# Optimization experiments

Hardware: AMD Instinct MI355X
Metric: run time of the kernel (lower is better)

Reference implementation:

```python
import jax, jax.numpy as jnp
import numpy as np

NUM_HEADS = 12

def setup_inputs() -> dict:
    key = jax.random.key(0)
    ks = jax.random.split(key, 8)
    B, C, H, W = 16, 512, 64, 64
    T = 768
    s = 0.02
    return {
        "cond": jax.random.normal(ks[0], (B, C, H, W), jnp.float32),
        "t": jax.random.normal(ks[1], (B, T), jnp.float32),
        "Wk": jax.random.normal(ks[2], (T, C), jnp.float32) * s,
        "bk": jax.random.normal(ks[3], (T,), jnp.float32) * s,
        "Wv": jax.random.normal(ks[4], (T, C), jnp.float32) * s,
        "bv": jax.random.normal(ks[5], (T,), jnp.float32) * s,
        "Wo": jax.random.normal(ks[6], (C, T), jnp.float32) * s,
        "bo": jax.random.normal(ks[7], (C,), jnp.float32) * s,
    }

def reference(cond, t, Wk, bk, Wv, bv, Wo, bo):
    B, C, H, W = cond.shape
    T = Wk.shape[0]
    h = NUM_HEADS
    d = T // h
    HW = H * W
    x = cond.reshape(B, C, HW)                                  # [B,C,HW]
    # 1x1 convs == channel GEMMs
    k = (jnp.einsum('tc,bcm->btm', Wk, x) + bk[None, :, None]).reshape(B, h, d, HW)
    v = (jnp.einsum('tc,bcm->btm', Wv, x) + bv[None, :, None]).reshape(B, h, d, HW)
    q = t.reshape(B, h, d)                                      # single query per head
    scale = d ** 0.5
    attn = jax.nn.softmax(jnp.einsum('bhd,bhdm->bhm', q, k) / scale, axis=-1)
    out = jnp.einsum('bhm,bhdm->bhd', attn, v).reshape(B, T)    # [B,T]
    out = jnp.einsum('ct,bt->bc', Wo, out) + bo                 # out_proj on (B,T,1,1)
    out = out[:, :, None, None]                                 # broadcast over H,W
    return out + cond
```

## Files before the change

kernel.cpp:

```cpp
#include <hip/hip_runtime.h>
#include <math.h>

#define B_   16
#define C_   512
#define HW_  4096
#define T_   768
#define NH   12
#define DH   64

typedef float nfloat4 __attribute__((ext_vector_type(4)));


__global__ __launch_bounds__(512) void qk_kernel(
    const float* __restrict__ t, const float* __restrict__ Wk,
    const float* __restrict__ bk, float* __restrict__ qkT,
    float* __restrict__ qb) {
  int bh = blockIdx.x;
  int b = bh / NH, h = bh % NH;
  __shared__ float tl[DH];
  int tid = threadIdx.x;
  if (tid < DH) tl[tid] = t[b * T_ + h * DH + tid];
  __syncthreads();
  int c = tid;
  float acc = 0.f;
#pragma unroll
  for (int dd = 0; dd < DH; ++dd)
    acc += tl[dd] * Wk[(h * DH + dd) * C_ + c];
  qkT[((size_t)b * C_ + c) * NH + h] = acc * 0.125f;
  if (tid == 0) {
    float s = 0.f;
    for (int dd = 0; dd < DH; ++dd) s += tl[dd] * bk[h * DH + dd];
    qb[bh] = s * 0.125f;
  }
}

template <int CS>
__global__ __launch_bounds__(128) void s_kernel(
    const float* __restrict__ x, const float* __restrict__ qkT,
    float* __restrict__ sp) {
  constexpr int CB = C_ / CS;
  int mt = blockIdx.x;
  int cs = blockIdx.y;
  int b  = blockIdx.z;
  int tid = threadIdx.x;

  __shared__ float qc[CB * NH];
  const float* src = qkT + ((size_t)b * C_ + cs * CB) * NH;
  for (int i = tid; i < CB * NH; i += 128) qc[i] = src[i];
  __syncthreads();

  int m0 = mt * 512 + tid * 4;
  float4 acc[NH];
#pragma unroll
  for (int h = 0; h < NH; ++h) acc[h] = make_float4(0.f, 0.f, 0.f, 0.f);

  const float* xb = x + (size_t)b * C_ * HW_ + (size_t)(cs * CB) * HW_ + m0;
  for (int c0 = 0; c0 < CB; c0 += 16) {
    float4 xv[16];
#pragma unroll
    for (int j = 0; j < 16; ++j)
      xv[j] = *(const float4*)(xb + (size_t)(c0 + j) * HW_);
#pragma unroll
    for (int j = 0; j < 16; ++j) {
      const float* q = qc + (c0 + j) * NH;
#pragma unroll
      for (int h = 0; h < NH; ++h) {
        float qh = q[h];
        acc[h].x += qh * xv[j].x; acc[h].y += qh * xv[j].y;
        acc[h].z += qh * xv[j].z; acc[h].w += qh * xv[j].w;
      }
    }
  }
  float* spp = sp + ((size_t)cs * B_ * NH + (size_t)b * NH) * HW_ + m0;
#pragma unroll
  for (int h = 0; h < NH; ++h)
    *(float4*)(spp + (size_t)h * HW_) = acc[h];
}

template <int CS>
__global__ __launch_bounds__(1024) void softmax_kernel(
    const float* __restrict__ sp, const float* __restrict__ qb,
    float* __restrict__ attn) {
  int bh = blockIdx.x;
  int tid = threadIdx.x;
  float qbv = qb[bh];
  const size_t S4 = (size_t)B_ * NH * (HW_ / 4);
  const float4* p = (const float4*)sp + (size_t)bh * (HW_ / 4) + tid;

  float4 v = make_float4(qbv, qbv, qbv, qbv);
#pragma unroll
  for (int s = 0; s < CS; ++s) {
    float4 pv = p[s * S4];
    v.x += pv.x; v.y += pv.y; v.z += pv.z; v.w += pv.w;
  }

  float vmax = fmaxf(fmaxf(v.x, v.y), fmaxf(v.z, v.w));
  for (int off = 32; off; off >>= 1) vmax = fmaxf(vmax, __shfl_xor(vmax, off));
  __shared__ float redm[16], reds[16];
  int w = tid >> 6;
  if ((tid & 63) == 0) redm[w] = vmax;
  __syncthreads();
  vmax = redm[0];
#pragma unroll
  for (int i = 1; i < 16; ++i) vmax = fmaxf(vmax, redm[i]);

  v.x = __expf(v.x - vmax); v.y = __expf(v.y - vmax);
  v.z = __expf(v.z - vmax); v.w = __expf(v.w - vmax);
  float sum = v.x + v.y + v.z + v.w;
  for (int off = 32; off; off >>= 1) sum += __shfl_xor(sum, off);
  if ((tid & 63) == 0) reds[w] = sum;
  __syncthreads();
  float tot = reds[0];
#pragma unroll
  for (int i = 1; i < 16; ++i) tot += reds[i];
  float inv = 1.f / tot;
  v.x *= inv; v.y *= inv; v.z *= inv; v.w *= inv;
  ((float4*)attn)[(size_t)bh * (HW_ / 4) + tid] = v;
}

__global__ __launch_bounds__(256) void y_kernel(
    const float* __restrict__ x, const float* __restrict__ attn,
    float* __restrict__ y) {
  int cg = blockIdx.x;
  int b  = blockIdx.y;
  int tid = threadIdx.x;
  int c0 = cg * 4;

  float acc[4][NH] = {};
  const float4* xb = (const float4*)(x + (size_t)b * C_ * HW_ + (size_t)c0 * HW_);
  const float4* ab = (const float4*)(attn + (size_t)b * NH * HW_);
#pragma unroll 1
  for (int k = 0; k < 4; ++k) {
    int m4 = k * 256 + tid;
    float4 xv[4];
#pragma unroll
    for (int g = 0; g < 4; ++g) xv[g] = xb[(size_t)g * (HW_ / 4) + m4];
    float4 a[NH];
#pragma unroll
    for (int h = 0; h < NH; ++h) a[h] = ab[(size_t)h * (HW_ / 4) + m4];
#pragma unroll
    for (int g = 0; g < 4; ++g)
#pragma unroll
      for (int h = 0; h < NH; ++h)
        acc[g][h] += a[h].x * xv[g].x + a[h].y * xv[g].y +
                     a[h].z * xv[g].z + a[h].w * xv[g].w;
  }
#pragma unroll
  for (int g = 0; g < 4; ++g)
#pragma unroll
    for (int h = 0; h < NH; ++h)
      for (int off = 32; off; off >>= 1)
        acc[g][h] += __shfl_xor(acc[g][h], off);

  __shared__ float red[4][48];
  int w = tid >> 6, lane = tid & 63;
  if (lane == 0) {
#pragma unroll
    for (int g = 0; g < 4; ++g)
#pragma unroll
      for (int h = 0; h < NH; ++h) red[w][g * NH + h] = acc[g][h];
  }
  __syncthreads();
  if (tid < 48) {
    float s = red[0][tid] + red[1][tid] + red[2][tid] + red[3][tid];
    int g = tid / NH, h = tid % NH;
    y[((size_t)b * NH + h) * C_ + c0 + g] = s;
  }
}

__global__ __launch_bounds__(256) void out_kernel(
    const float* __restrict__ Wv, const float* __restrict__ bv,
    const float* __restrict__ y, float* __restrict__ outT) {
  int o = blockIdx.x * 4 + (threadIdx.x >> 6);
  int lane = threadIdx.x & 63;
  int b = o / T_, t = o % T_;
  int h = t / DH;
  const float* wr = Wv + (size_t)t * C_;
  const float* yr = y + ((size_t)b * NH + h) * C_;
  float s = 0.f;
#pragma unroll
  for (int j = 0; j < 8; ++j) { int c = j * 64 + lane; s += wr[c] * yr[c]; }
  for (int off = 32; off; off >>= 1) s += __shfl_xor(s, off);
  if (lane == 0) outT[o] = s + bv[t];
}

__global__ __launch_bounds__(256) void z_kernel(
    const float* __restrict__ Wo, const float* __restrict__ bo,
    const float* __restrict__ outT, float* __restrict__ z) {
  int o = blockIdx.x * 4 + (threadIdx.x >> 6);
  int lane = threadIdx.x & 63;
  int b = o / C_, c = o % C_;
  const float* wr = Wo + (size_t)c * T_;
  const float* orr = outT + (size_t)b * T_;
  float s = 0.f;
#pragma unroll
  for (int j = 0; j < 12; ++j) { int t = j * 64 + lane; s += wr[t] * orr[t]; }
  for (int off = 32; off; off >>= 1) s += __shfl_xor(s, off);
  if (lane == 0) z[o] = s + bo[c];
}

__global__ __launch_bounds__(256) void add_kernel(
    const float* __restrict__ cond, const float* __restrict__ z,
    float* __restrict__ out) {
  size_t i0 = (size_t)blockIdx.x * 512 + threadIdx.x;
  size_t i1 = i0 + 256;
  nfloat4 c0 = __builtin_nontemporal_load(&((const nfloat4*)cond)[i0]);
  nfloat4 c1 = __builtin_nontemporal_load(&((const nfloat4*)cond)[i1]);
  float z0 = z[(int)(i0 >> 10)];
  float z1 = z[(int)(i1 >> 10)];
  nfloat4 r0 = c0 + z0;
  nfloat4 r1 = c1 + z1;
  __builtin_nontemporal_store(r0, &((nfloat4*)out)[i0]);
  __builtin_nontemporal_store(r1, &((nfloat4*)out)[i1]);
}

template <int CS>
static void run_pipeline(const float* cond, const float* t, const float* Wk,
                         const float* bk, const float* Wv, const float* bv,
                         const float* Wo, const float* bo, float* out,
                         float* ws, int out_size, hipStream_t stream) {
  float* qkT  = ws;
  float* qb   = ws + 98304;
  float* sp   = ws + 98496;
  float* attn = sp + (size_t)CS * 786432;
  float* y    = attn + 786432;
  float* outT = y + 98304;
  float* z    = outT + 12288;

  hipLaunchKernelGGL(qk_kernel, dim3(B_ * NH), dim3(512), 0, stream,
                     t, Wk, bk, qkT, qb);
  hipLaunchKernelGGL((s_kernel<CS>), dim3(8, CS, B_), dim3(128), 0, stream,
                     cond, qkT, sp);
  hipLaunchKernelGGL((softmax_kernel<CS>), dim3(B_ * NH), dim3(1024), 0, stream,
                     sp, qb, attn);
  hipLaunchKernelGGL(y_kernel, dim3(128, B_), dim3(256), 0, stream,
                     cond, attn, y);
  hipLaunchKernelGGL(out_kernel, dim3((B_ * T_) / 4), dim3(256), 0, stream,
                     Wv, bv, y, outT);
  hipLaunchKernelGGL(z_kernel, dim3((B_ * C_) / 4), dim3(256), 0, stream,
                     Wo, bo, outT, z);
  hipLaunchKernelGGL(add_kernel, dim3(out_size / 4 / 512), dim3(256), 0,
                     stream, cond, z, out);
}

extern "C" void kernel_launch(void* const* d_in, const int* in_sizes, int n_in,
                              void* d_out, int out_size, void* d_ws, size_t ws_size,
                              hipStream_t stream) {
  const float* cond = (const float*)d_in[0];
  const float* t    = (const float*)d_in[1];
  const float* Wk   = (const float*)d_in[2];
  const float* bk   = (const float*)d_in[3];
  const float* Wv   = (const float*)d_in[4];
  const float* bv   = (const float*)d_in[5];
  const float* Wo   = (const float*)d_in[6];
  const float* bo   = (const float*)d_in[7];
  float* out = (float*)d_out;
  float* ws  = (float*)d_ws;

  const size_t need8 = (size_t)(98496 + 8 * 786432 + 786432 + 98304 + 12288 + 8192) * 4;
  if (ws_size >= need8) {
    run_pipeline<8>(cond, t, Wk, bk, Wv, bv, Wo, bo, out, ws, out_size, stream);
  } else {
    run_pipeline<4>(cond, t, Wk, bk, Wv, bv, Wo, bo, out, ws, out_size, stream);
  }
}
```

Measured before the change: 322.6 us.

## Fuse the whole multi-kernel pipeline into one cooperative persistent kernel

```diff
diff --git a/kernel.cpp b/kernel.cpp
--- a/kernel.cpp
+++ b/kernel.cpp
@@ -1,5 +1,8 @@
 #include <hip/hip_runtime.h>
+#include <hip/hip_cooperative_groups.h>
 #include <math.h>
+
+namespace cg = cooperative_groups;
 
 #define B_   16
 #define C_   512
@@ -10,6 +13,248 @@
 
 typedef float nfloat4 __attribute__((ext_vector_type(4)));
 
+
+template <int CS>
+__global__ __launch_bounds__(256, 4) void mega_kernel(
+    const float* __restrict__ cond, const float* __restrict__ tvec,
+    const float* __restrict__ Wk, const float* __restrict__ bk,
+    const float* __restrict__ Wv, const float* __restrict__ bv,
+    const float* __restrict__ Wo, const float* __restrict__ bo,
+    float* __restrict__ out, float* __restrict__ ws) {
+  constexpr int CB = C_ / CS;
+  float* qkT  = ws;
+  float* qb   = ws + 98304;
+  float* sp   = ws + 98496;
+  float* attn = sp + (size_t)CS * 786432;
+  float* y    = attn + 786432;
+  float* outT = y + 98304;
+  float* z    = outT + 12288;
+  const float* x = cond;
+
+  cg::grid_group grid = cg::this_grid();
+  const int tid = threadIdx.x;
+  const int nb  = gridDim.x;
+
+  __shared__ float lds[1536];
+
+  for (int u = blockIdx.x; u < B_ * NH; u += nb) {
+    int b = u / NH, h = u % NH;
+    if (tid < DH) lds[tid] = tvec[b * T_ + h * DH + tid];
+    __syncthreads();
+#pragma unroll
+    for (int cc = 0; cc < 2; ++cc) {
+      int c = cc * 256 + tid;
+      float acc = 0.f;
+#pragma unroll
+      for (int dd = 0; dd < DH; ++dd)
+        acc += lds[dd] * Wk[(h * DH + dd) * C_ + c];
+      qkT[((size_t)b * C_ + c) * NH + h] = acc * 0.125f;
+    }
+    if (tid == 0) {
+      float s = 0.f;
+      for (int dd = 0; dd < DH; ++dd) s += lds[dd] * bk[h * DH + dd];
+      qb[u] = s * 0.125f;
+    }
+    __syncthreads();
+  }
+  grid.sync();
+
+  for (int u = blockIdx.x; u < 8 * CS * B_; u += nb) {
+    int mt = u & 7;
+    int cs = (u >> 3) % CS;
+    int b  = u / (8 * CS);
+    const float* src = qkT + ((size_t)b * C_ + cs * CB) * NH;
+    for (int i = tid; i < CB * NH; i += 256) lds[i] = src[i];
+    __syncthreads();
+    int m0 = mt * 512 + tid * 2;
+    float ax[NH], ay[NH];
+#pragma unroll
+    for (int h = 0; h < NH; ++h) { ax[h] = 0.f; ay[h] = 0.f; }
+    const float* xb = x + (size_t)b * C_ * HW_ + (size_t)(cs * CB) * HW_ + m0;
+    for (int c0 = 0; c0 < CB; c0 += 16) {
+      float2 xv[16];
+#pragma unroll
+      for (int j = 0; j < 16; ++j)
+        xv[j] = *(const float2*)(xb + (size_t)(c0 + j) * HW_);
+#pragma unroll
+      for (int j = 0; j < 16; ++j) {
+        const float4* q4 = (const float4*)(lds + (c0 + j) * NH);
+        float4 qa = q4[0], qb2 = q4[1], qc2 = q4[2];
+        ax[0] += qa.x * xv[j].x;  ay[0] += qa.x * xv[j].y;
+        ax[1] += qa.y * xv[j].x;  ay[1] += qa.y * xv[j].y;
+        ax[2] += qa.z * xv[j].x;  ay[2] += qa.z * xv[j].y;
+        ax[3] += qa.w * xv[j].x;  ay[3] += qa.w * xv[j].y;
+        ax[4] += qb2.x * xv[j].x; ay[4] += qb2.x * xv[j].y;
+        ax[5] += qb2.y * xv[j].x; ay[5] += qb2.y * xv[j].y;
+        ax[6] += qb2.z * xv[j].x; ay[6] += qb2.z * xv[j].y;
+        ax[7] += qb2.w * xv[j].x; ay[7] += qb2.w * xv[j].y;
+        ax[8] += qc2.x * xv[j].x; ay[8] += qc2.x * xv[j].y;
+        ax[9] += qc2.y * xv[j].x; ay[9] += qc2.y * xv[j].y;
+        ax[10] += qc2.z * xv[j].x; ay[10] += qc2.z * xv[j].y;
+        ax[11] += qc2.w * xv[j].x; ay[11] += qc2.w * xv[j].y;
+      }
+    }
+    float* spp = sp + ((size_t)cs * B_ * NH + (size_t)b * NH) * HW_ + m0;
+#pragma unroll
+    for (int h = 0; h < NH; ++h) {
+      float2 v; v.x = ax[h]; v.y = ay[h];
+      *(float2*)(spp + (size_t)h * HW_) = v;
+    }
+    __syncthreads();
+  }
+  grid.sync();
+
+  for (int u = blockIdx.x; u < B_ * NH; u += nb) {
+    float qbv = qb[u];
+    const size_t S4 = (size_t)B_ * NH * (HW_ / 4);
+    const float4* p = (const float4*)sp + (size_t)u * (HW_ / 4);
+    float4 v[4];
+#pragma unroll
+    for (int k = 0; k < 4; ++k) {
+      int idx = k * 256 + tid;
+      float4 vv = make_float4(qbv, qbv, qbv, qbv);
+#pragma unroll
+      for (int s = 0; s < CS; ++s) {
+        float4 pv = p[(size_t)s * S4 + idx];
+        vv.x += pv.x; vv.y += pv.y; vv.z += pv.z; vv.w += pv.w;
+      }
+      v[k] = vv;
+    }
+    float vmax = -1e30f;
+#pragma unroll
+    for (int k = 0; k < 4; ++k)
+      vmax = fmaxf(vmax, fmaxf(fmaxf(v[k].x, v[k].y), fmaxf(v[k].z, v[k].w)));
+    for (int off = 32; off; off >>= 1) vmax = fmaxf(vmax, __shfl_xor(vmax, off));
+    if ((tid & 63) == 0) lds[tid >> 6] = vmax;
+    __syncthreads();
+    vmax = fmaxf(fmaxf(lds[0], lds[1]), fmaxf(lds[2], lds[3]));
+    float sum = 0.f;
+#pragma unroll
+    for (int k = 0; k < 4; ++k) {
+      v[k].x = __expf(v[k].x - vmax); v[k].y = __expf(v[k].y - vmax);
+      v[k].z = __expf(v[k].z - vmax); v[k].w = __expf(v[k].w - vmax);
+      sum += v[k].x + v[k].y + v[k].z + v[k].w;
+    }
+    for (int off = 32; off; off >>= 1) sum += __shfl_xor(sum, off);
+    if ((tid & 63) == 0) lds[4 + (tid >> 6)] = sum;
+    __syncthreads();
+    float inv = 1.f / (lds[4] + lds[5] + lds[6] + lds[7]);
+    float4* ap = (float4*)attn + (size_t)u * (HW_ / 4);
+#pragma unroll
+    for (int k = 0; k < 4; ++k) {
+      int idx = k * 256 + tid;
+      float4 vv = v[k];
+      vv.x *= inv; vv.y *= inv; vv.z *= inv; vv.w *= inv;
+      ap[idx] = vv;
+    }
+    __syncthreads();
+  }
+  grid.sync();
+
+  for (int u = blockIdx.x; u < 128 * B_; u += nb) {
+    int cgrp = u & 127;
+    int b = u >> 7;
+    int c0 = cgrp * 4;
+    float acc[4][NH];
+#pragma unroll
+    for (int g = 0; g < 4; ++g)
+#pragma unroll
+      for (int h = 0; h < NH; ++h) acc[g][h] = 0.f;
+    const float4* xb = (const float4*)(x + (size_t)b * C_ * HW_ + (size_t)c0 * HW_);
+    const float4* ab = (const float4*)(attn + (size_t)b * NH * HW_);
+#pragma unroll 1
+    for (int k = 0; k < 4; ++k) {
+      int m4 = k * 256 + tid;
+      float4 xv[4];
+#pragma unroll
+      for (int g = 0; g < 4; ++g) xv[g] = xb[(size_t)g * (HW_ / 4) + m4];
+#pragma unroll
+      for (int hh = 0; hh < NH; hh += 4) {
+        float4 a[4];
+#pragma unroll
+        for (int h = 0; h < 4; ++h) a[h] = ab[(size_t)(hh + h) * (HW_ / 4) + m4];
+#pragma unroll
+        for (int g = 0; g < 4; ++g)
+#pragma unroll
+          for (int h = 0; h < 4; ++h)
+            acc[g][hh + h] += a[h].x * xv[g].x + a[h].y * xv[g].y +
+                              a[h].z * xv[g].z + a[h].w * xv[g].w;
+      }
+    }
+#pragma unroll
+    for (int g = 0; g < 4; ++g)
+#pragma unroll
+      for (int h = 0; h < NH; ++h)
+        for (int off = 32; off; off >>= 1)
+          acc[g][h] += __shfl_xor(acc[g][h], off);
+    int w = tid >> 6, lane = tid & 63;
+    if (lane == 0) {
+#pragma unroll
+      for (int g = 0; g < 4; ++g)
+#pragma unroll
+        for (int h = 0; h < NH; ++h) lds[w * 48 + g * NH + h] = acc[g][h];
+    }
+    __syncthreads();
+    if (tid < 48) {
+      float s = lds[tid] + lds[48 + tid] + lds[96 + tid] + lds[144 + tid];
+      int g = tid / NH, h = tid % NH;
+      y[((size_t)b * NH + h) * C_ + c0 + g] = s;
+    }
+    __syncthreads();
+  }
+  grid.sync();
+
+  for (int u = blockIdx.x; u < (B_ * T_) / 4; u += nb) {
+    int o = u * 4 + (tid >> 6);
+    int lane = tid & 63;
+    int b = o / T_, to = o % T_;
+    int h = to / DH;
+    const float* wr = Wv + (size_t)to * C_;
+    const float* yr = y + ((size_t)b * NH + h) * C_;
+    float s = 0.f;
+#pragma unroll
+    for (int j = 0; j < 8; ++j) { int c = j * 64 + lane; s += wr[c] * yr[c]; }
+    for (int off = 32; off; off >>= 1) s += __shfl_xor(s, off);
+    if (lane == 0) outT[o] = s + bv[to];
+  }
+  grid.sync();
+
+  for (int u = blockIdx.x; u < (B_ * C_) / 4; u += nb) {
+    int o = u * 4 + (tid >> 6);
+    int lane = tid & 63;
+    int b = o / C_, c = o % C_;
+    const float* wr = Wo + (size_t)c * T_;
+    const float* orr = outT + (size_t)b * T_;
+    float s = 0.f;
+#pragma unroll
+    for (int j = 0; j < 12; ++j) { int t2 = j * 64 + lane; s += wr[t2] * orr[t2]; }
+    for (int off = 32; off; off >>= 1) s += __shfl_xor(s, off);
+    if (lane == 0) z[o] = s + bo[c];
+  }
+  grid.sync();
+
+  {
+    const size_t total4 = (size_t)B_ * C_ * HW_ / 4;
+    const size_t stride = (size_t)nb * 256;
+    size_t i = (size_t)blockIdx.x * 256 + tid;
+    for (; i + 3 * stride < total4; i += 4 * stride) {
+      size_t i1 = i + stride, i2 = i + 2 * stride, i3 = i + 3 * stride;
+      nfloat4 c0v = __builtin_nontemporal_load(&((const nfloat4*)cond)[i]);
+      nfloat4 c1v = __builtin_nontemporal_load(&((const nfloat4*)cond)[i1]);
+      nfloat4 c2v = __builtin_nontemporal_load(&((const nfloat4*)cond)[i2]);
+      nfloat4 c3v = __builtin_nontemporal_load(&((const nfloat4*)cond)[i3]);
+      float z0 = z[i >> 10], z1 = z[i1 >> 10], z2 = z[i2 >> 10], z3 = z[i3 >> 10];
+      __builtin_nontemporal_store(c0v + z0, &((nfloat4*)out)[i]);
+      __builtin_nontemporal_store(c1v + z1, &((nfloat4*)out)[i1]);
+      __builtin_nontemporal_store(c2v + z2, &((nfloat4*)out)[i2]);
+      __builtin_nontemporal_store(c3v + z3, &((nfloat4*)out)[i3]);
+    }
+    for (; i < total4; i += stride) {
+      nfloat4 cv = __builtin_nontemporal_load(&((const nfloat4*)cond)[i]);
+      __builtin_nontemporal_store(cv + z[i >> 10], &((nfloat4*)out)[i]);
+    }
+  }
+}
 
 __global__ __launch_bounds__(512) void qk_kernel(
     const float* __restrict__ t, const float* __restrict__ Wk,
@@ -258,9 +503,41 @@
   float* ws  = (float*)d_ws;
 
   const size_t need8 = (size_t)(98496 + 8 * 786432 + 786432 + 98304 + 12288 + 8192) * 4;
-  if (ws_size >= need8) {
-    run_pipeline<8>(cond, t, Wk, bk, Wv, bv, Wo, bo, out, ws, out_size, stream);
+  const bool use8 = ws_size >= need8;
+
+  static int nb8 = -2, nb4 = -2;
+  if (nb8 == -2) {
+    int dev = 0, coop = 0, ncu = 256;
+    hipGetDevice(&dev);
+    hipDeviceGetAttribute(&coop, hipDeviceAttributeCooperativeLaunch, dev);
+    hipDeviceGetAttribute(&ncu, hipDeviceAttributeMultiprocessorCount, dev);
+    if (ncu <= 0) ncu = 256;
+    if (coop) {
+      int m8 = 0, m4 = 0;
+      hipError_t e1 = hipOccupancyMaxActiveBlocksPerMultiprocessor(&m8, mega_kernel<8>, 256, 0);
+      hipError_t e2 = hipOccupancyMaxActiveBlocksPerMultiprocessor(&m4, mega_kernel<4>, 256, 0);
+      nb8 = (e1 == hipSuccess && m8 >= 1)
+                ? ((m8 * ncu > 2048) ? 2048 : m8 * ncu) : -1;
+      nb4 = (e2 == hipSuccess && m4 >= 1)
+                ? ((m4 * ncu > 2048) ? 2048 : m4 * ncu) : -1;
+    } else {
+      nb8 = -1; nb4 = -1;
+    }
+  }
+
+  int nb = use8 ? nb8 : nb4;
+  if (nb > 0) {
+    void* args[] = {(void*)&cond, (void*)&t, (void*)&Wk, (void*)&bk,
+                    (void*)&Wv, (void*)&bv, (void*)&Wo, (void*)&bo,
+                    (void*)&out, (void*)&ws};
+    if (use8)
+      hipLaunchCooperativeKernel(mega_kernel<8>, dim3(nb), dim3(256), args, 0, stream);
+    else
+      hipLaunchCooperativeKernel(mega_kernel<4>, dim3(nb), dim3(256), args, 0, stream);
   } else {
-    run_pipeline<4>(cond, t, Wk, bk, Wv, bv, Wo, bo, out, ws, out_size, stream);
-  }
-}
+    if (use8)
+      run_pipeline<8>(cond, t, Wk, bk, Wv, bv, Wo, bo, out, ws, out_size, stream);
+    else
+      run_pipeline<4>(cond, t, Wk, bk, Wv, bv, Wo, bo, out, ws, out_size, stream);
+  }
+}
```

Result: slower. 658.5 us (+104.1%).
